# Optimization experiments

Hardware: AMD Instinct MI355X
Metric: run time of the kernel (lower is better)

The kernel has to match this reference:

```python
import jax, jax.numpy as jnp
import numpy as np

V, D, S, B = 16384, 384, 512, 128
H, HD = 6, 64
DIN, DFF = 768, 1536
NM, NA = 6, 2
EPS = 1e-5


def _ln(x, w, b):
    mu = jnp.mean(x, axis=-1, keepdims=True)
    var = jnp.mean((x - mu) ** 2, axis=-1, keepdims=True)
    return (x - mu) * jax.lax.rsqrt(var + EPS) * w + b


def setup_inputs() -> dict:
    key = jax.random.key(0)
    ks = iter(jax.random.split(key, 40))
    g = lambda shape, s=0.02: (jax.random.normal(next(ks), shape, dtype=jnp.float32) * s)
    emb = g((V, D)).at[0].set(0.0)  # padding_idx=0
    inp = {
        'input_ids': jax.random.randint(next(ks), (B, S), 0, V, dtype=jnp.int32),
        'emb': emb,
        'pos_emb': g((S, D)),
        # 6 Mamba-fallback blocks (stacked)
        'm_ln_w': jnp.ones((NM, D), jnp.float32), 'm_ln_b': jnp.zeros((NM, D), jnp.float32),
        'm_W1': g((NM, D, DIN)), 'm_b1': jnp.zeros((NM, DIN), jnp.float32),
        'm_W2': g((NM, DIN, D)), 'm_b2': jnp.zeros((NM, D), jnp.float32),
        # 2 transformer encoder layers (stacked), post-norm, ReLU FFN
        'a_qkv_w': g((NA, D, 3 * D)), 'a_qkv_b': jnp.zeros((NA, 3 * D), jnp.float32),
        'a_out_w': g((NA, D, D)), 'a_out_b': jnp.zeros((NA, D), jnp.float32),
        'a_ln1_w': jnp.ones((NA, D), jnp.float32), 'a_ln1_b': jnp.zeros((NA, D), jnp.float32),
        'a_ln2_w': jnp.ones((NA, D), jnp.float32), 'a_ln2_b': jnp.zeros((NA, D), jnp.float32),
        'a_ff_w1': g((NA, D, DFF)), 'a_ff_b1': jnp.zeros((NA, DFF), jnp.float32),
        'a_ff_w2': g((NA, DFF, D)), 'a_ff_b2': jnp.zeros((NA, D), jnp.float32),
        'fn_w': jnp.ones((D,), jnp.float32), 'fn_b': jnp.zeros((D,), jnp.float32),
        'h_w1': g((D, 128)), 'h_b1': jnp.zeros((128,), jnp.float32),
        'h_w2': g((128, 1)), 'h_b2': jnp.zeros((1,), jnp.float32),
    }
    return inp


def _forward(input_ids, emb, pos_emb, m_ln_w, m_ln_b, m_W1, m_b1, m_W2, m_b2,
             a_qkv_w, a_qkv_b, a_out_w, a_out_b, a_ln1_w, a_ln1_b, a_ln2_w, a_ln2_b,
             a_ff_w1, a_ff_b1, a_ff_w2, a_ff_b2, fn_w, fn_b, h_w1, h_b1, h_w2, h_b2):
    x = emb[input_ids] + pos_emb[None, :input_ids.shape[1], :]  # (B,S,D)
    # 6 residual Mamba-fallback blocks: x + W2(silu(W1(ln(x))))
    for i in range(NM):
        h = _ln(x, m_ln_w[i], m_ln_b[i])
        h = jax.nn.silu(h @ m_W1[i] + m_b1[i]) @ m_W2[i] + m_b2[i]
        x = x + h
    # 2 post-norm transformer encoder layers
    scale = 1.0 / np.sqrt(HD)
    for i in range(NA):
        qkv = x @ a_qkv_w[i] + a_qkv_b[i]
        q, k, v = jnp.split(qkv, 3, axis=-1)
        q = q.reshape(*q.shape[:2], H, HD)
        k = k.reshape(*k.shape[:2], H, HD)
        v = v.reshape(*v.shape[:2], H, HD)
        scores = jnp.einsum('bqhd,bkhd->bhqk', q, k) * scale
        attn = jax.nn.softmax(scores, axis=-1)
        o = jnp.einsum('bhqk,bkhd->bqhd', attn, v).reshape(x.shape)
        o = o @ a_out_w[i] + a_out_b[i]
        x = _ln(x + o, a_ln1_w[i], a_ln1_b[i])
        f = jax.nn.relu(x @ a_ff_w1[i] + a_ff_b1[i]) @ a_ff_w2[i] + a_ff_b2[i]
        x = _ln(x + f, a_ln2_w[i], a_ln2_b[i])
    x = _ln(x, fn_w, fn_b)
    cls = x[:, 0, :]
    return jax.nn.relu(cls @ h_w1 + h_b1) @ h_w2 + h_b2  # (B,1)


def reference(input_ids, emb, pos_emb, m_ln_w, m_ln_b, m_W1, m_b1, m_W2, m_b2,
              a_qkv_w, a_qkv_b, a_out_w, a_out_b, a_ln1_w, a_ln1_b, a_ln2_w, a_ln2_b,
              a_ff_w1, a_ff_b1, a_ff_w2, a_ff_b2, fn_w, fn_b, h_w1, h_b1, h_w2, h_b2):
    return _forward(input_ids, emb, pos_emb, m_ln_w, m_ln_b, m_W1, m_b1, m_W2, m_b2,
                    a_qkv_w, a_qkv_b, a_out_w, a_out_b, a_ln1_w, a_ln1_b, a_ln2_w, a_ln2_b,
                    a_ff_w1, a_ff_b1, a_ff_w2, a_ff_b2, fn_w, fn_b, h_w1, h_b1, h_w2, h_b2)
```

## Files before the change

### kernel.cpp

```cpp
#include <hip/hip_runtime.h>
#include <hip/hip_bf16.h>
#include <math.h>

#define B_   128
#define S_   512
#define D_   384
#define H_   6
#define HD_  64
#define DIN_ 768
#define DFF_ 1536
#define NM_  6
#define NA_  2
#define EPS_ 1e-5f

typedef __hip_bfloat16 bf16;
typedef __attribute__((ext_vector_type(8))) short short8;
typedef __attribute__((ext_vector_type(4))) float f32x4;

__device__ __forceinline__ float bf2f(unsigned short u) {
    union { unsigned int i; float f; } c; c.i = ((unsigned int)u) << 16; return c.f;
}

__device__ __forceinline__ void async16(const void* g, void* l) {
    __builtin_amdgcn_global_load_lds((const __attribute__((address_space(1))) void*)g,
                                     (__attribute__((address_space(3))) void*)l, 16, 0, 0);
}

__global__ __launch_bounds__(128) void embed_kernel(const int* __restrict__ ids,
    const float* __restrict__ emb, const float* __restrict__ pos,
    float* __restrict__ x)
{
    int row = blockIdx.x;
    int id  = ids[row];
    int s   = row & (S_ - 1);
    const float* e = emb + (size_t)id * D_;
    const float* p = pos + (size_t)s * D_;
    float* xr = x + (size_t)row * D_;
    for (int d = threadIdx.x; d < D_; d += 128) xr[d] = e[d] + p[d];
}

__global__ __launch_bounds__(128) void ln_kernel(const float* __restrict__ src,
    const float* __restrict__ res, const float* __restrict__ w,
    const float* __restrict__ bias, float* __restrict__ outf, bf16* __restrict__ outb)
{
    int row = blockIdx.x;
    const float* sr = src + (size_t)row * D_;
    int tid = threadIdx.x;
    float v[3];
    float s = 0.f, ss = 0.f;
    #pragma unroll
    for (int i = 0; i < 3; ++i) {
        int d = tid + i * 128;
        float t = sr[d];
        if (res) t += res[(size_t)row * D_ + d];
        v[i] = t; s += t; ss += t * t;
    }
    #pragma unroll
    for (int off = 32; off > 0; off >>= 1) {
        s  += __shfl_down(s, off);
        ss += __shfl_down(ss, off);
    }
    __shared__ float red[2][2];
    int wave = tid >> 6, lane = tid & 63;
    if (lane == 0) { red[wave][0] = s; red[wave][1] = ss; }
    __syncthreads();
    float S0 = red[0][0] + red[1][0];
    float SS = red[0][1] + red[1][1];
    float mu  = S0 * (1.f / D_);
    float var = SS * (1.f / D_) - mu * mu;
    float rs  = rsqrtf(var + EPS_);
    #pragma unroll
    for (int i = 0; i < 3; ++i) {
        int d = tid + i * 128;
        float o = (v[i] - mu) * rs * w[d] + bias[d];
        if (outf) outf[(size_t)row * D_ + d] = o;
        if (outb) outb[(size_t)row * D_ + d] = __float2bfloat16(o);
    }
}

__global__ __launch_bounds__(128) void ln_cls_kernel(const float* __restrict__ x,
    const float* __restrict__ w, const float* __restrict__ bias, float* __restrict__ cls)
{
    int b = blockIdx.x;
    const float* sr = x + (size_t)b * S_ * D_;
    int tid = threadIdx.x;
    float v[3];
    float s = 0.f, ss = 0.f;
    #pragma unroll
    for (int i = 0; i < 3; ++i) {
        int d = tid + i * 128;
        float t = sr[d];
        v[i] = t; s += t; ss += t * t;
    }
    #pragma unroll
    for (int off = 32; off > 0; off >>= 1) {
        s  += __shfl_down(s, off);
        ss += __shfl_down(ss, off);
    }
    __shared__ float red[2][2];
    int wave = tid >> 6, lane = tid & 63;
    if (lane == 0) { red[wave][0] = s; red[wave][1] = ss; }
    __syncthreads();
    float S0 = red[0][0] + red[1][0];
    float SS = red[0][1] + red[1][1];
    float mu  = S0 * (1.f / D_);
    float var = SS * (1.f / D_) - mu * mu;
    float rs  = rsqrtf(var + EPS_);
    #pragma unroll
    for (int i = 0; i < 3; ++i) {
        int d = tid + i * 128;
        cls[(size_t)b * D_ + d] = (v[i] - mu) * rs * w[d] + bias[d];
    }
}

__global__ __launch_bounds__(256) void cvt_kernel(const float* __restrict__ x,
                                                  bf16* __restrict__ xb)
{
    int i = (blockIdx.x * 256 + threadIdx.x) * 4;
    float4 v = *(const float4*)(x + i);
    bf16* o = xb + i;
    o[0] = __float2bfloat16(v.x); o[1] = __float2bfloat16(v.y);
    o[2] = __float2bfloat16(v.z); o[3] = __float2bfloat16(v.w);
}

__global__ __launch_bounds__(256) void wcvt_kernel(const float* __restrict__ W,
    bf16* __restrict__ Wt, int K, int N)
{
    __shared__ float tile[32][33];
    int tid = threadIdx.x;
    int tx = tid & 31, ty = tid >> 5;
    int n0 = blockIdx.x * 32, k0 = blockIdx.y * 32;
    #pragma unroll
    for (int i = 0; i < 4; ++i)
        tile[ty + i * 8][tx] = W[(size_t)(k0 + ty + i * 8) * N + n0 + tx];
    __syncthreads();
    #pragma unroll
    for (int i = 0; i < 4; ++i)
        Wt[(size_t)(n0 + ty + i * 8) * K + k0 + tx] = __float2bfloat16(tile[tx][ty + i * 8]);
}

__global__ __launch_bounds__(256) void gemm_bf16(
    const bf16* __restrict__ A, const bf16* __restrict__ Bt,
    const float* __restrict__ bias, const float* __restrict__ R,
    float* __restrict__ Cf, bf16* __restrict__ Cb,
    int N, int K, int act)
{
    __shared__ __align__(16) short As[2][4096];
    __shared__ __align__(16) short Bs[2][4096];
    const int tid  = threadIdx.x;
    const int wave = tid >> 6, lane = tid & 63;
    const int m0 = blockIdx.y * 128;
    const int n0 = blockIdx.x * 128;
    const int lr = lane & 15, lk = lane >> 4;
    const int wm = wave >> 1, wn = wave & 1;

    const bf16* Ab = A  + (size_t)m0 * K;
    const bf16* Bb = Bt + (size_t)n0 * K;

    const int st_row  = (wave * 2) * 16 + (lane >> 2);
    const int st_col0 = (lane & 3);

    f32x4 acc[4][4];
    #pragma unroll
    for (int i = 0; i < 4; ++i)
        #pragma unroll
        for (int j = 0; j < 4; ++j)
            acc[i][j] = (f32x4){0.f, 0.f, 0.f, 0.f};

    const int KT = K >> 5;

    #pragma unroll
    for (int j = 0; j < 2; ++j) {
        int row = st_row + j * 16;
        int ks  = st_col0 ^ (row & 3);
        int chunk = wave * 2 + j;
        async16(Ab + (size_t)row * K + ks * 8, &As[0][chunk * 512]);
        async16(Bb + (size_t)row * K + ks * 8, &Bs[0][chunk * 512]);
    }

    for (int kt = 0; kt < KT; ++kt) {
        const int cur = kt & 1;
        __syncthreads();
        if (kt + 1 < KT) {
            const int k0 = (kt + 1) << 5;
            #pragma unroll
            for (int j = 0; j < 2; ++j) {
                int row = st_row + j * 16;
                int ks  = st_col0 ^ (row & 3);
                int chunk = wave * 2 + j;
                async16(Ab + (size_t)row * K + k0 + ks * 8, &As[cur ^ 1][chunk * 512]);
                async16(Bb + (size_t)row * K + k0 + ks * 8, &Bs[cur ^ 1][chunk * 512]);
            }
        }
        short8 af[4], bfr[4];
        #pragma unroll
        for (int i = 0; i < 4; ++i) {
            int ra = wm * 64 + i * 16 + lr;
            af[i]  = *(const short8*)&As[cur][ra * 32 + ((lk ^ (ra & 3)) << 3)];
            int rb = wn * 64 + i * 16 + lr;
            bfr[i] = *(const short8*)&Bs[cur][rb * 32 + ((lk ^ (rb & 3)) << 3)];
        }
        #pragma unroll
        for (int mi = 0; mi < 4; ++mi)
            #pragma unroll
            for (int ni = 0; ni < 4; ++ni)
                acc[mi][ni] = __builtin_amdgcn_mfma_f32_16x16x32_bf16(af[mi], bfr[ni], acc[mi][ni], 0, 0, 0);
    }

    #pragma unroll
    for (int mi = 0; mi < 4; ++mi) {
        #pragma unroll
        for (int ni = 0; ni < 4; ++ni) {
            int col = n0 + wn * 64 + ni * 16 + lr;
            float bv = bias[col];
            #pragma unroll
            for (int j = 0; j < 4; ++j) {
                int row = m0 + wm * 64 + mi * 16 + lk * 4 + j;
                float t = acc[mi][ni][j] + bv;
                if (act == 1)      t = t / (1.f + __expf(-t));
                else if (act == 2) t = fmaxf(t, 0.f);
                size_t idx = (size_t)row * N + col;
                if (R)  t += R[idx];
                if (Cf) Cf[idx] = t;
                if (Cb) Cb[idx] = __float2bfloat16(t);
            }
        }
    }
}

__global__ __launch_bounds__(256) void attn_mfma(const bf16* __restrict__ qkv,
                                                 bf16* __restrict__ o)
{
    const int qb  = blockIdx.x;
    const int h   = blockIdx.y;
    const int b   = blockIdx.z;
    const int tid = threadIdx.x;
    const int wave = tid >> 6, lane = tid & 63;
    const int lr = lane & 15, lg = lane >> 4;

    __shared__ __align__(16) short Qs[4096];
    __shared__ __align__(16) short Ks[4096];
    __shared__ __align__(16) short Vts[4096];
    __shared__ __align__(16) short Ps[4][1024];

    const size_t baseRow = (size_t)b * S_;
    const bf16* gq = qkv + baseRow * 1152 + (size_t)h * 64;

    #pragma unroll
    for (int i = 0; i < 2; ++i) {
        int cid = i * 256 + tid;
        int r = cid >> 3, g = cid & 7;
        short8 v = *(const short8*)(gq + (size_t)(qb * 64 + r) * 1152 + g * 8);
        *(short8*)&Qs[r * 64 + ((g ^ (r & 7)) << 3)] = v;
    }

    f32x4 acc_o[4];
    #pragma unroll
    for (int i = 0; i < 4; ++i) acc_o[i] = (f32x4){0.f, 0.f, 0.f, 0.f};
    float m_run[4] = {-1e30f, -1e30f, -1e30f, -1e30f};
    float l_run[4] = {0.f, 0.f, 0.f, 0.f};

    for (int kt = 0; kt < 8; ++kt) {
        __syncthreads();
        #pragma unroll
        for (int i = 0; i < 2; ++i) {
            int cid = i * 256 + tid;
            int r = cid >> 3, g = cid & 7;
            short8 v = *(const short8*)(gq + 384 + (size_t)(kt * 64 + r) * 1152 + g * 8);
            *(short8*)&Ks[r * 64 + ((g ^ (r & 7)) << 3)] = v;
        }
        #pragma unroll
        for (int i = 0; i < 2; ++i) {
            int k  = tid & 63;
            int d0 = ((tid >> 6) << 3) + i * 32;
            short8 v = *(const short8*)(gq + 768 + (size_t)(kt * 64 + k) * 1152 + d0);
            #pragma unroll
            for (int j = 0; j < 8; ++j) {
                int d = d0 + j;
                Vts[d * 64 + (((k >> 3) ^ (d & 7)) << 3) + (k & 7)] = v[j];
            }
        }
        __syncthreads();

        f32x4 s[4];
        #pragma unroll
        for (int i = 0; i < 4; ++i) s[i] = (f32x4){0.f, 0.f, 0.f, 0.f};
        short8 qa0, qa1;
        {
            int r = wave * 16 + lr;
            qa0 = *(const short8*)&Qs[r * 64 + ((lg ^ (r & 7)) << 3)];
            qa1 = *(const short8*)&Qs[r * 64 + (((4 + lg) ^ (r & 7)) << 3)];
        }
        #pragma unroll
        for (int ks2 = 0; ks2 < 4; ++ks2) {
            int rk = ks2 * 16 + lr;
            short8 kb0 = *(const short8*)&Ks[rk * 64 + ((lg ^ (rk & 7)) << 3)];
            short8 kb1 = *(const short8*)&Ks[rk * 64 + (((4 + lg) ^ (rk & 7)) << 3)];
            s[ks2] = __builtin_amdgcn_mfma_f32_16x16x32_bf16(qa0, kb0, s[ks2], 0, 0, 0);
            s[ks2] = __builtin_amdgcn_mfma_f32_16x16x32_bf16(qa1, kb1, s[ks2], 0, 0, 0);
        }
        #pragma unroll
        for (int ks2 = 0; ks2 < 4; ++ks2)
            #pragma unroll
            for (int jj = 0; jj < 4; ++jj)
                s[ks2][jj] *= 0.125f;

        #pragma unroll
        for (int jj = 0; jj < 4; ++jj) {
            float tm = fmaxf(fmaxf(s[0][jj], s[1][jj]), fmaxf(s[2][jj], s[3][jj]));
            tm = fmaxf(tm, __shfl_xor(tm, 1));
            tm = fmaxf(tm, __shfl_xor(tm, 2));
            tm = fmaxf(tm, __shfl_xor(tm, 4));
            tm = fmaxf(tm, __shfl_xor(tm, 8));
            float mn = fmaxf(m_run[jj], tm);
            float resc = __expf(m_run[jj] - mn);
            m_run[jj] = mn;
            float rs = 0.f;
            #pragma unroll
            for (int ks2 = 0; ks2 < 4; ++ks2) {
                float p = __expf(s[ks2][jj] - mn);
                s[ks2][jj] = p;
                rs += p;
            }
            rs += __shfl_xor(rs, 1);
            rs += __shfl_xor(rs, 2);
            rs += __shfl_xor(rs, 4);
            rs += __shfl_xor(rs, 8);
            l_run[jj] = l_run[jj] * resc + rs;
            #pragma unroll
            for (int ds2 = 0; ds2 < 4; ++ds2) acc_o[ds2][jj] *= resc;
        }

        short* pw = &Ps[wave][0];
        #pragma unroll
        for (int ks2 = 0; ks2 < 4; ++ks2)
            #pragma unroll
            for (int jj = 0; jj < 4; ++jj) {
                int q = lg * 4 + jj;
                int k = ks2 * 16 + lr;
                bf16 pb = __float2bfloat16(s[ks2][jj]);
                pw[q * 64 + (((k >> 3) ^ (q & 7)) << 3) + (k & 7)] = *(short*)&pb;
            }
        short8 pa0 = *(const short8*)&pw[lr * 64 + ((lg ^ (lr & 7)) << 3)];
        short8 pa1 = *(const short8*)&pw[lr * 64 + (((4 + lg) ^ (lr & 7)) << 3)];

        #pragma unroll
        for (int ds2 = 0; ds2 < 4; ++ds2) {
            int d = ds2 * 16 + lr;
            short8 vb0 = *(const short8*)&Vts[d * 64 + ((lg ^ (d & 7)) << 3)];
            short8 vb1 = *(const short8*)&Vts[d * 64 + (((4 + lg) ^ (d & 7)) << 3)];
            acc_o[ds2] = __builtin_amdgcn_mfma_f32_16x16x32_bf16(pa0, vb0, acc_o[ds2], 0, 0, 0);
            acc_o[ds2] = __builtin_amdgcn_mfma_f32_16x16x32_bf16(pa1, vb1, acc_o[ds2], 0, 0, 0);
        }
    }

    #pragma unroll
    for (int jj = 0; jj < 4; ++jj) {
        float inv = 1.f / l_run[jj];
        size_t row = baseRow + qb * 64 + wave * 16 + lg * 4 + jj;
        #pragma unroll
        for (int ds2 = 0; ds2 < 4; ++ds2)
            o[row * 384 + h * 64 + ds2 * 16 + lr] = __float2bfloat16(acc_o[ds2][jj] * inv);
    }
}

__global__ __launch_bounds__(128) void head_kernel(const float* __restrict__ cls,
    const float* __restrict__ w1, const float* __restrict__ b1,
    const float* __restrict__ w2, const float* __restrict__ b2,
    float* __restrict__ out)
{
    int b = blockIdx.x;
    int tid = threadIdx.x;
    __shared__ float c[384];
    const float* xr = cls + (size_t)b * 384;
    for (int d = tid; d < 384; d += 128) c[d] = xr[d];
    __syncthreads();
    float hacc = b1[tid];
    for (int k = 0; k < 384; ++k) hacc += c[k] * w1[k * 128 + tid];
    hacc = fmaxf(hacc, 0.f);
    float p = hacc * w2[tid];
    #pragma unroll
    for (int off = 32; off > 0; off >>= 1) p += __shfl_down(p, off);
    __shared__ float r2[2];
    if ((tid & 63) == 0) r2[tid >> 6] = p;
    __syncthreads();
    if (tid == 0) out[b] = r2[0] + r2[1] + b2[0];
}

extern "C" void kernel_launch(void* const* d_in, const int* in_sizes, int n_in,
                              void* d_out, int out_size, void* d_ws, size_t ws_size,
                              hipStream_t stream)
{
    const int*   ids     = (const int*)d_in[0];
    const float* emb     = (const float*)d_in[1];
    const float* pos     = (const float*)d_in[2];
    const float* m_ln_w  = (const float*)d_in[3];
    const float* m_ln_b  = (const float*)d_in[4];
    const float* m_W1    = (const float*)d_in[5];
    const float* m_b1    = (const float*)d_in[6];
    const float* m_W2    = (const float*)d_in[7];
    const float* m_b2    = (const float*)d_in[8];
    const float* a_qkv_w = (const float*)d_in[9];
    const float* a_qkv_b = (const float*)d_in[10];
    const float* a_out_w = (const float*)d_in[11];
    const float* a_out_b = (const float*)d_in[12];
    const float* a_ln1_w = (const float*)d_in[13];
    const float* a_ln1_b = (const float*)d_in[14];
    const float* a_ln2_w = (const float*)d_in[15];
    const float* a_ln2_b = (const float*)d_in[16];
    const float* a_ff_w1 = (const float*)d_in[17];
    const float* a_ff_b1 = (const float*)d_in[18];
    const float* a_ff_w2 = (const float*)d_in[19];
    const float* a_ff_b2 = (const float*)d_in[20];
    const float* fn_w    = (const float*)d_in[21];
    const float* fn_b    = (const float*)d_in[22];
    const float* h_w1    = (const float*)d_in[23];
    const float* h_b1    = (const float*)d_in[24];
    const float* h_w2    = (const float*)d_in[25];
    const float* h_b2    = (const float*)d_in[26];
    float* out = (float*)d_out;

    const size_t M = (size_t)B_ * S_;
    const size_t WBYTES = 7077888ull * 2;

    int NC = 8;
    {
        const int cand[4] = {1, 2, 4, 8};
        for (int ci = 0; ci < 4; ++ci) {
            size_t mc = M / cand[ci];
            size_t need = M * 1536 + mc * 6144 + WBYTES + 1024;
            if (need <= ws_size) { NC = cand[ci]; break; }
        }
    }
    const size_t MC = M / NC;
    const int    BC = (int)(MC / S_);

    char* wp = (char*)d_ws;
    float* x    = (float*)wp;               wp += M  * 384 * 4;
    float* t0   = (float*)wp;               wp += MC * 384 * 4;
    bf16*  xcb  = (bf16*)wp;                wp += MC * 384 * 2;
    bf16*  midb = (bf16*)wp;                wp += MC * 1536 * 2;
    bf16*  t2b  = (bf16*)wp;                wp += MC * 384 * 2;
    bf16*  Wt   = (bf16*)wp;

    bf16* mW1t = Wt;
    bf16* mW2t = mW1t + 6 * 768 * 384;
    bf16* qkvt = mW2t + 6 * 384 * 768;
    bf16* outt = qkvt + 2 * 1152 * 384;
    bf16* ff1t = outt + 2 * 384 * 384;
    bf16* ff2t = ff1t + 2 * 1536 * 384;

    for (int i = 0; i < NM_; ++i) {
        wcvt_kernel<<<dim3(DIN_ / 32, D_ / 32), 256, 0, stream>>>(m_W1 + (size_t)i * D_ * DIN_, mW1t + (size_t)i * DIN_ * D_, D_, DIN_);
        wcvt_kernel<<<dim3(D_ / 32, DIN_ / 32), 256, 0, stream>>>(m_W2 + (size_t)i * DIN_ * D_, mW2t + (size_t)i * D_ * DIN_, DIN_, D_);
    }
    for (int i = 0; i < NA_; ++i) {
        wcvt_kernel<<<dim3(1152 / 32, D_ / 32), 256, 0, stream>>>(a_qkv_w + (size_t)i * D_ * 1152, qkvt + (size_t)i * 1152 * D_, D_, 1152);
        wcvt_kernel<<<dim3(D_ / 32, D_ / 32), 256, 0, stream>>>(a_out_w + (size_t)i * D_ * D_, outt + (size_t)i * D_ * D_, D_, D_);
        wcvt_kernel<<<dim3(DFF_ / 32, D_ / 32), 256, 0, stream>>>(a_ff_w1 + (size_t)i * D_ * DFF_, ff1t + (size_t)i * DFF_ * D_, D_, DFF_);
        wcvt_kernel<<<dim3(D_ / 32, DFF_ / 32), 256, 0, stream>>>(a_ff_w2 + (size_t)i * DFF_ * D_, ff2t + (size_t)i * D_ * DFF_, DFF_, D_);
    }

    embed_kernel<<<(int)M, 128, 0, stream>>>(ids, emb, pos, x);

    const int GM = (int)(MC / 128);

    for (int i = 0; i < NM_; ++i) {
        for (int c = 0; c < NC; ++c) {
            float* xc = x + (size_t)c * MC * 384;
            ln_kernel<<<(int)MC, 128, 0, stream>>>(xc, nullptr, m_ln_w + i * D_, m_ln_b + i * D_, nullptr, xcb);
            gemm_bf16<<<dim3(DIN_ / 128, GM), 256, 0, stream>>>(
                xcb, mW1t + (size_t)i * DIN_ * D_, m_b1 + i * DIN_, nullptr, nullptr, midb, DIN_, D_, 1);
            gemm_bf16<<<dim3(D_ / 128, GM), 256, 0, stream>>>(
                midb, mW2t + (size_t)i * D_ * DIN_, m_b2 + i * D_, xc, xc, nullptr, D_, DIN_, 0);
        }
    }
    for (int i = 0; i < NA_; ++i) {
        for (int c = 0; c < NC; ++c) {
            float* xc = x + (size_t)c * MC * 384;
            cvt_kernel<<<(int)(MC * 384 / 1024), 256, 0, stream>>>(xc, xcb);
            gemm_bf16<<<dim3(1152 / 128, GM), 256, 0, stream>>>(
                xcb, qkvt + (size_t)i * 1152 * D_, a_qkv_b + i * 1152, nullptr, nullptr, midb, 1152, D_, 0);
            attn_mfma<<<dim3(S_ / 64, H_, BC), 256, 0, stream>>>(midb, t2b);
            gemm_bf16<<<dim3(D_ / 128, GM), 256, 0, stream>>>(
                t2b, outt + (size_t)i * D_ * D_, a_out_b + i * D_, nullptr, t0, nullptr, D_, D_, 0);
            ln_kernel<<<(int)MC, 128, 0, stream>>>(xc, t0, a_ln1_w + i * D_, a_ln1_b + i * D_, xc, xcb);
            gemm_bf16<<<dim3(DFF_ / 128, GM), 256, 0, stream>>>(
                xcb, ff1t + (size_t)i * DFF_ * D_, a_ff_b1 + i * DFF_, nullptr, nullptr, midb, DFF_, D_, 2);
            gemm_bf16<<<dim3(D_ / 128, GM), 256, 0, stream>>>(
                midb, ff2t + (size_t)i * D_ * DFF_, a_ff_b2 + i * D_, nullptr, t0, nullptr, D_, DFF_, 0);
            ln_kernel<<<(int)MC, 128, 0, stream>>>(xc, t0, a_ln2_w + i * D_, a_ln2_b + i * D_, xc, nullptr);
        }
    }
    ln_cls_kernel<<<B_, 128, 0, stream>>>(x, fn_w, fn_b, t0);
    head_kernel<<<B_, 128, 0, stream>>>(t0, h_w1, h_b1, h_w2, h_b2, out);
}
```

Measured before the change: 4.075 ms.

## Emit bf16 activations from GEMM epilogues and drop separate conversion kernel

The last Mamba block's W2 GEMM and the attention LN2 now also write a bf16 copy of the residual stream, so the fp32-to-bf16 cvt_kernel before each QKV GEMM is removed. The out-projection and FFN2 GEMMs write their pre-LN results in bf16 instead of fp32, halving that intermediate traffic, and LN reads the bf16 residual. Per-layer weight conversion launches are batched using blockIdx.z, and the attention output buffer is aliased into midb. The bf16 residual input to LayerNorm adds rounding error compared with the fp32 path.

```diff
diff --git a/kernel.cpp b/kernel.cpp
--- a/kernel.cpp
+++ b/kernel.cpp
@@ -40,7 +40,7 @@
 }
 
 __global__ __launch_bounds__(128) void ln_kernel(const float* __restrict__ src,
-    const float* __restrict__ res, const float* __restrict__ w,
+    const bf16* __restrict__ res, const float* __restrict__ w,
     const float* __restrict__ bias, float* __restrict__ outf, bf16* __restrict__ outb)
 {
     int row = blockIdx.x;
@@ -52,7 +52,7 @@
     for (int i = 0; i < 3; ++i) {
         int d = tid + i * 128;
         float t = sr[d];
-        if (res) t += res[(size_t)row * D_ + d];
+        if (res) t += __bfloat162float(res[(size_t)row * D_ + d]);
         v[i] = t; s += t; ss += t * t;
     }
     #pragma unroll
@@ -113,19 +113,11 @@
     }
 }
 
-__global__ __launch_bounds__(256) void cvt_kernel(const float* __restrict__ x,
-                                                  bf16* __restrict__ xb)
-{
-    int i = (blockIdx.x * 256 + threadIdx.x) * 4;
-    float4 v = *(const float4*)(x + i);
-    bf16* o = xb + i;
-    o[0] = __float2bfloat16(v.x); o[1] = __float2bfloat16(v.y);
-    o[2] = __float2bfloat16(v.z); o[3] = __float2bfloat16(v.w);
-}
-
 __global__ __launch_bounds__(256) void wcvt_kernel(const float* __restrict__ W,
     bf16* __restrict__ Wt, int K, int N)
 {
+    W  += (size_t)blockIdx.z * K * N;
+    Wt += (size_t)blockIdx.z * N * K;
     __shared__ float tile[32][33];
     int tid = threadIdx.x;
     int tx = tid & 31, ty = tid >> 5;
@@ -428,7 +420,7 @@
         const int cand[4] = {1, 2, 4, 8};
         for (int ci = 0; ci < 4; ++ci) {
             size_t mc = M / cand[ci];
-            size_t need = M * 1536 + mc * 6144 + WBYTES + 1024;
+            size_t need = M * 1536 + M * 768 + mc * 4608 + WBYTES + 4096;
             if (need <= ws_size) { NC = cand[ci]; break; }
         }
     }
@@ -437,11 +429,12 @@
 
     char* wp = (char*)d_ws;
     float* x    = (float*)wp;               wp += M  * 384 * 4;
-    float* t0   = (float*)wp;               wp += MC * 384 * 4;
+    bf16*  xb   = (bf16*)wp;                wp += M  * 384 * 2;
     bf16*  xcb  = (bf16*)wp;                wp += MC * 384 * 2;
     bf16*  midb = (bf16*)wp;                wp += MC * 1536 * 2;
-    bf16*  t2b  = (bf16*)wp;                wp += MC * 384 * 2;
+    bf16*  t0b  = (bf16*)wp;                wp += MC * 384 * 2;
     bf16*  Wt   = (bf16*)wp;
+    bf16*  t2b  = midb + MC * 1152;
 
     bf16* mW1t = Wt;
     bf16* mW2t = mW1t + 6 * 768 * 384;
@@ -450,16 +443,12 @@
     bf16* ff1t = outt + 2 * 384 * 384;
     bf16* ff2t = ff1t + 2 * 1536 * 384;
 
-    for (int i = 0; i < NM_; ++i) {
-        wcvt_kernel<<<dim3(DIN_ / 32, D_ / 32), 256, 0, stream>>>(m_W1 + (size_t)i * D_ * DIN_, mW1t + (size_t)i * DIN_ * D_, D_, DIN_);
-        wcvt_kernel<<<dim3(D_ / 32, DIN_ / 32), 256, 0, stream>>>(m_W2 + (size_t)i * DIN_ * D_, mW2t + (size_t)i * D_ * DIN_, DIN_, D_);
-    }
-    for (int i = 0; i < NA_; ++i) {
-        wcvt_kernel<<<dim3(1152 / 32, D_ / 32), 256, 0, stream>>>(a_qkv_w + (size_t)i * D_ * 1152, qkvt + (size_t)i * 1152 * D_, D_, 1152);
-        wcvt_kernel<<<dim3(D_ / 32, D_ / 32), 256, 0, stream>>>(a_out_w + (size_t)i * D_ * D_, outt + (size_t)i * D_ * D_, D_, D_);
-        wcvt_kernel<<<dim3(DFF_ / 32, D_ / 32), 256, 0, stream>>>(a_ff_w1 + (size_t)i * D_ * DFF_, ff1t + (size_t)i * DFF_ * D_, D_, DFF_);
-        wcvt_kernel<<<dim3(D_ / 32, DFF_ / 32), 256, 0, stream>>>(a_ff_w2 + (size_t)i * DFF_ * D_, ff2t + (size_t)i * D_ * DFF_, DFF_, D_);
-    }
+    wcvt_kernel<<<dim3(DIN_ / 32, D_ / 32, NM_), 256, 0, stream>>>(m_W1, mW1t, D_, DIN_);
+    wcvt_kernel<<<dim3(D_ / 32, DIN_ / 32, NM_), 256, 0, stream>>>(m_W2, mW2t, DIN_, D_);
+    wcvt_kernel<<<dim3(1152 / 32, D_ / 32, NA_), 256, 0, stream>>>(a_qkv_w, qkvt, D_, 1152);
+    wcvt_kernel<<<dim3(D_ / 32, D_ / 32, NA_), 256, 0, stream>>>(a_out_w, outt, D_, D_);
+    wcvt_kernel<<<dim3(DFF_ / 32, D_ / 32, NA_), 256, 0, stream>>>(a_ff_w1, ff1t, D_, DFF_);
+    wcvt_kernel<<<dim3(D_ / 32, DFF_ / 32, NA_), 256, 0, stream>>>(a_ff_w2, ff2t, DFF_, D_);
 
     embed_kernel<<<(int)M, 128, 0, stream>>>(ids, emb, pos, x);
 
@@ -467,31 +456,35 @@
 
     for (int i = 0; i < NM_; ++i) {
         for (int c = 0; c < NC; ++c) {
-            float* xc = x + (size_t)c * MC * 384;
+            float* xc  = x  + (size_t)c * MC * 384;
+            bf16*  xbc = xb + (size_t)c * MC * 384;
             ln_kernel<<<(int)MC, 128, 0, stream>>>(xc, nullptr, m_ln_w + i * D_, m_ln_b + i * D_, nullptr, xcb);
             gemm_bf16<<<dim3(DIN_ / 128, GM), 256, 0, stream>>>(
                 xcb, mW1t + (size_t)i * DIN_ * D_, m_b1 + i * DIN_, nullptr, nullptr, midb, DIN_, D_, 1);
             gemm_bf16<<<dim3(D_ / 128, GM), 256, 0, stream>>>(
-                midb, mW2t + (size_t)i * D_ * DIN_, m_b2 + i * D_, xc, xc, nullptr, D_, DIN_, 0);
+                midb, mW2t + (size_t)i * D_ * DIN_, m_b2 + i * D_, xc, xc,
+                (i == NM_ - 1) ? xbc : nullptr, D_, DIN_, 0);
         }
     }
     for (int i = 0; i < NA_; ++i) {
         for (int c = 0; c < NC; ++c) {
-            float* xc = x + (size_t)c * MC * 384;
-            cvt_kernel<<<(int)(MC * 384 / 1024), 256, 0, stream>>>(xc, xcb);
+            float* xc  = x  + (size_t)c * MC * 384;
+            bf16*  xbc = xb + (size_t)c * MC * 384;
             gemm_bf16<<<dim3(1152 / 128, GM), 256, 0, stream>>>(
-                xcb, qkvt + (size_t)i * 1152 * D_, a_qkv_b + i * 1152, nullptr, nullptr, midb, 1152, D_, 0);
+                xbc, qkvt + (size_t)i * 1152 * D_, a_qkv_b + i * 1152, nullptr, nullptr, midb, 1152, D_, 0);
             attn_mfma<<<dim3(S_ / 64, H_, BC), 256, 0, stream>>>(midb, t2b);
             gemm_bf16<<<dim3(D_ / 128, GM), 256, 0, stream>>>(
-                t2b, outt + (size_t)i * D_ * D_, a_out_b + i * D_, nullptr, t0, nullptr, D_, D_, 0);
-            ln_kernel<<<(int)MC, 128, 0, stream>>>(xc, t0, a_ln1_w + i * D_, a_ln1_b + i * D_, xc, xcb);
+                t2b, outt + (size_t)i * D_ * D_, a_out_b + i * D_, nullptr, nullptr, t0b, D_, D_, 0);
+            ln_kernel<<<(int)MC, 128, 0, stream>>>(xc, t0b, a_ln1_w + i * D_, a_ln1_b + i * D_, xc, xcb);
             gemm_bf16<<<dim3(DFF_ / 128, GM), 256, 0, stream>>>(
                 xcb, ff1t + (size_t)i * DFF_ * D_, a_ff_b1 + i * DFF_, nullptr, nullptr, midb, DFF_, D_, 2);
             gemm_bf16<<<dim3(D_ / 128, GM), 256, 0, stream>>>(
-                midb, ff2t + (size_t)i * D_ * DFF_, a_ff_b2 + i * D_, nullptr, t0, nullptr, D_, DFF_, 0);
-            ln_kernel<<<(int)MC, 128, 0, stream>>>(xc, t0, a_ln2_w + i * D_, a_ln2_b + i * D_, xc, nullptr);
-        }
-    }
-    ln_cls_kernel<<<B_, 128, 0, stream>>>(x, fn_w, fn_b, t0);
-    head_kernel<<<B_, 128, 0, stream>>>(t0, h_w1, h_b1, h_w2, h_b2, out);
-}
+                midb, ff2t + (size_t)i * D_ * DFF_, a_ff_b2 + i * D_, nullptr, nullptr, t0b, D_, DFF_, 0);
+            ln_kernel<<<(int)MC, 128, 0, stream>>>(xc, t0b, a_ln2_w + i * D_, a_ln2_b + i * D_, xc,
+                                                   (i + 1 < NA_) ? xbc : nullptr);
+        }
+    }
+    ln_cls_kernel<<<B_, 128, 0, stream>>>(x, fn_w, fn_b, (float*)((char*)d_ws + M * 384 * 4 + M * 384 * 2));
+    head_kernel<<<B_, 128, 0, stream>>>((const float*)((char*)d_ws + M * 384 * 4 + M * 384 * 2),
+                                        h_w1, h_b1, h_w2, h_b2, out);
+}
```

New measurement: 3.978 ms. 2.4% less time.
